# Optimization experiments

Measured on AMD Instinct MI355X. Metric: run time of the kernel, lower is better.

## Reference

```python
import jax, jax.numpy as jnp
import numpy as np

# Config (matches BlockConfig defaults for linear attention)
B, S, D = 2, 4096, 2048
H, KVH, HD, CK = 16, 8, 128, 4   # n_heads, n_kv_heads, head_dim, conv_kernel
DQK, DV = KVH * HD, H * HD       # 1024, 2048
EPS = 1e-6


def setup_inputs() -> dict:
    key = jax.random.key(0)
    ks = jax.random.split(key, 12)
    std = 0.02
    return {
        "x": jax.random.normal(ks[0], (B, S, D), jnp.float32),
        "wq": jax.random.normal(ks[1], (DQK, D), jnp.float32) * std,
        "wk": jax.random.normal(ks[2], (DQK, D), jnp.float32) * std,
        "wv": jax.random.normal(ks[3], (DV, D), jnp.float32) * std,
        "wo": jax.random.normal(ks[4], (D, DV), jnp.float32) * std,
        "q_conv_w": jax.random.normal(ks[5], (DQK, 1, CK), jnp.float32) * std,
        "k_conv_w": jax.random.normal(ks[6], (DQK, 1, CK), jnp.float32) * std,
        "alpha_w": jax.random.normal(ks[7], (H, D), jnp.float32) * std,
        "alpha_b": jnp.zeros((H,), jnp.float32),
        "beta_w": jax.random.normal(ks[8], (H, D), jnp.float32) * std,
        "beta_b": jnp.zeros((H,), jnp.float32),
        "g_w": jax.random.normal(ks[9], (DV, D), jnp.float32) * std,
        "norm_q_w": jnp.ones((HD,), jnp.float32),
        "norm_k_w": jnp.ones((HD,), jnp.float32),
    }


def _rmsnorm(x, w):
    # normalize over last dim (head_dim) in fp32, elementwise affine, no bias
    xf = x.astype(jnp.float32)
    var = jnp.mean(xf * xf, axis=-1, keepdims=True)
    return (w * xf * jax.lax.rsqrt(var + EPS)).astype(x.dtype)


def _causal_dwconv(x, w):
    # x: (B, S, C); w: (C, 1, k) depthwise; torch Conv1d padding=k-1 then [:S]
    # == left-pad (k-1, 0) cross-correlation
    y = jax.lax.conv_general_dilated(
        x.transpose(0, 2, 1), w, window_strides=(1,),
        padding=[(CK - 1, 0)], feature_group_count=w.shape[0],
        dimension_numbers=("NCH", "OIH", "NCH"))
    return y.transpose(0, 2, 1)


def reference(x, wq, wk, wv, wo, q_conv_w, k_conv_w,
              alpha_w, alpha_b, beta_w, beta_b, g_w, norm_q_w, norm_k_w):
    Q = x @ wq.T                              # (B,S,DQK)
    K = x @ wk.T                              # (B,S,DQK)
    V = x @ wv.T                              # (B,S,DV)
    Q = _causal_dwconv(Q, q_conv_w)
    K = _causal_dwconv(K, k_conv_w)
    Q = _rmsnorm(Q.reshape(B, S, KVH, HD), norm_q_w)
    K = _rmsnorm(K.reshape(B, S, KVH, HD), norm_k_w)
    V = V.reshape(B, S, H, HD)
    alpha = jax.nn.sigmoid(x @ alpha_w.T + alpha_b)              # (B,S,H)
    beta = jax.nn.sigmoid(x @ beta_w.T + beta_b) / (HD ** 0.5)   # (B,S,H)
    rep = H // KVH
    Q = jnp.repeat(Q, rep, axis=2)            # (B,S,H,HD)
    K = jnp.repeat(K, rep, axis=2)

    # time-major for scan
    Qt = Q.transpose(1, 0, 2, 3)
    Kt = K.transpose(1, 0, 2, 3)
    Vt = V.transpose(1, 0, 2, 3)
    at = alpha.transpose(1, 0, 2)
    bt = beta.transpose(1, 0, 2)

    S0 = jnp.zeros((B, H, HD, HD), x.dtype)

    def step(S_state, inp):
        q_t, k_t, v_t, a_t, b_t = inp
        pred = jnp.einsum("bhd,bhdv->bhv", k_t, S_state)
        delta = v_t - pred
        update = jnp.einsum("bhv,bhd->bhdv", delta, k_t)
        S_state = a_t[:, :, None, None] * S_state + b_t[:, :, None, None] * update
        o_t = jnp.einsum("bhd,bhdv->bhv", q_t, S_state)
        return S_state, o_t

    _, O = jax.lax.scan(step, S0, (Qt, Kt, Vt, at, bt))  # O: (S,B,H,HD)
    out = O.transpose(1, 0, 2, 3).reshape(B, S, DV)
    g = jax.nn.sigmoid(x @ g_w.T)
    return (g * out) @ wo.T
```

## Files before the change

### kernel.cpp

```cpp
#include <hip/hip_runtime.h>
#include <stdint.h>

#define DEV static __device__ __forceinline__

typedef __bf16 bf16x8 __attribute__((ext_vector_type(8)));
typedef float f32x4 __attribute__((ext_vector_type(4)));

constexpr int Bc = 2, Sc = 4096, Dc = 2048, Hc = 16, KVHc = 8, HDc = 128;
constexpr int DQKc = 1024, DVc = 2048;
constexpr int Mc = Bc * Sc;
constexpr int NCATc = 6144;
constexpr int CT = 64;
constexpr int NCH = Sc / CT;
constexpr int COEF_STRIDE = 25088;
constexpr float EPSc = 1e-6f;

DEV uint16_t f2bf(float f) {
  uint32_t u = __float_as_uint(f);
  u += 0x7FFFu + ((u >> 16) & 1u);
  return (uint16_t)(u >> 16);
}
DEV float bf2f(uint16_t h) { return __uint_as_float(((uint32_t)h) << 16); }
DEV float sigmoidf_(float z) { return 1.0f / (1.0f + __expf(-z)); }

DEV void unpack8(uint4 u, float* f) {
  f[0] = __uint_as_float(u.x << 16); f[1] = __uint_as_float(u.x & 0xFFFF0000u);
  f[2] = __uint_as_float(u.y << 16); f[3] = __uint_as_float(u.y & 0xFFFF0000u);
  f[4] = __uint_as_float(u.z << 16); f[5] = __uint_as_float(u.z & 0xFFFF0000u);
  f[6] = __uint_as_float(u.w << 16); f[7] = __uint_as_float(u.w & 0xFFFF0000u);
}

DEV void gload16(void* lds, const void* g) {
  auto gp = (const __attribute__((address_space(1))) uint32_t*)(uintptr_t)g;
  auto lp = (__attribute__((address_space(3))) uint32_t*)(uint32_t)(uintptr_t)lds;
  __builtin_amdgcn_global_load_lds(gp, lp, 16, 0, 0);
}

DEV void sync_lds() {
  asm volatile("s_waitcnt lgkmcnt(0)" ::: "memory");
  __builtin_amdgcn_sched_barrier(0);
  __builtin_amdgcn_s_barrier();
  __builtin_amdgcn_sched_barrier(0);
}

__global__ __launch_bounds__(256) void cast6_kernel(const float* __restrict__ x,
                                                    const float* __restrict__ wq,
                                                    const float* __restrict__ wk,
                                                    const float* __restrict__ wv,
                                                    const float* __restrict__ gw,
                                                    const float* __restrict__ wo,
                                                    uint16_t* __restrict__ xb,
                                                    uint16_t* __restrict__ wcat,
                                                    uint16_t* __restrict__ wob) {
  int i = blockIdx.x * blockDim.x + threadIdx.x;
  const int stride = gridDim.x * blockDim.x;
  for (; i < 8388608; i += stride) {
    const float* src;
    uint16_t* dst;
    int off;
    if (i < 4194304)      { src = x;  dst = xb;                     off = i; }
    else if (i < 4718592) { src = wq; dst = wcat;                   off = i - 4194304; }
    else if (i < 5242880) { src = wk; dst = wcat + DQKc * Dc;       off = i - 4718592; }
    else if (i < 6291456) { src = wv; dst = wcat + 2 * DQKc * Dc;   off = i - 5242880; }
    else if (i < 7340032) { src = gw; dst = wcat + 2 * DQKc * Dc + DVc * Dc; off = i - 6291456; }
    else                  { src = wo; dst = wob;                    off = i - 7340032; }
    float4 v = *(const float4*)(src + (size_t)off * 4);
    ushort4 o;
    o.x = f2bf(v.x); o.y = f2bf(v.y); o.z = f2bf(v.z); o.w = f2bf(v.w);
    *(ushort4*)(dst + (size_t)off * 4) = o;
  }
}

template <typename OutT>
__global__ __launch_bounds__(512, 2) void gemm256_bt(const uint16_t* __restrict__ A,
                                                     const uint16_t* __restrict__ Bw,
                                                     OutT* __restrict__ C, int Ndim, int Kdim,
                                                     int lda) {
  __shared__ uint16_t sT[2][2][2][8192];

  const int nbn = Ndim / 256;
  const int cpx = nbn >> 3;
  const int xcd = blockIdx.x & 7, lin = blockIdx.x >> 3;
  const int bn = xcd * cpx + lin % cpx;
  const int bm = lin / cpx;

  const int tid = threadIdx.x;
  const int wid = tid >> 6, lane = tid & 63;
  const int wm = wid >> 2, wn = wid & 3;
  const int lr = lane & 15;
  const int sswz8 = (((lane >> 4) ^ ((lr >> 1) & 3)) * 8);
  const int arow_base = wm * 128 + lr;
  const int brow_base = wn * 64 + lr;

  const uint16_t* Ab = A + (size_t)(bm * 256) * lda;
  const uint16_t* Bb = Bw + (size_t)(bn * 256) * Kdim;
  const int NT = Kdim >> 6;

  int srowA[2];
  int soff[2];
  const int wbase = tid & ~63;
#pragma unroll
  for (int u = 0; u < 2; ++u) {
    int L = u * 512 + tid;
    srowA[u] = L >> 2;
    soff[u] = (((L & 3) ^ ((L >> 3) & 3)) * 8);
  }

  auto STAGE = [&](int buf, int mat, int kh, int kt) {
    const uint16_t* gb = mat == 0 ? Ab : Bb;
    const int ld = mat == 0 ? lda : Kdim;
    uint16_t* rg = &sT[buf][mat][kh][0];
#pragma unroll
    for (int u = 0; u < 2; ++u) {
      const uint16_t* g = gb + (size_t)srowA[u] * ld + kt * 64 + kh * 32 + soff[u];
      gload16(rg + (u * 512 + wbase) * 8, g);
    }
  };

  f32x4 acc[8][4] = {};
  bf16x8 bfr[4];

  STAGE(0, 0, 0, 0); STAGE(0, 1, 0, 0);
  STAGE(0, 0, 1, 0); STAGE(0, 1, 1, 0);
  STAGE(1, 0, 0, 1); STAGE(1, 1, 0, 1);
  asm volatile("s_waitcnt vmcnt(4)" ::: "memory");
  __builtin_amdgcn_s_barrier();

  for (int kt = 0; kt < NT; ++kt) {
    const int buf = kt & 1;
    const uint16_t* aR0 = &sT[buf][0][0][0];
    const uint16_t* bR0 = &sT[buf][1][0][0];
    const uint16_t* aR1 = &sT[buf][0][1][0];
    const uint16_t* bR1 = &sT[buf][1][1][0];

    {
      bf16x8 af[4];
#pragma unroll
      for (int m = 0; m < 4; ++m)
        af[m] = *(const bf16x8*)&aR0[(arow_base + m * 16) * 32 + sswz8];
#pragma unroll
      for (int n = 0; n < 4; ++n)
        bfr[n] = *(const bf16x8*)&bR0[(brow_base + n * 16) * 32 + sswz8];
      if (kt + 1 < NT) STAGE(buf ^ 1, 0, 1, kt + 1);
      __builtin_amdgcn_s_setprio(1);
#pragma unroll
      for (int m = 0; m < 4; ++m)
#pragma unroll
        for (int n = 0; n < 4; ++n)
          acc[m][n] = __builtin_amdgcn_mfma_f32_16x16x32_bf16(af[m], bfr[n], acc[m][n], 0, 0, 0);
      __builtin_amdgcn_s_setprio(0);
      __builtin_amdgcn_s_barrier();
    }
    {
      bf16x8 af[4];
#pragma unroll
      for (int m = 0; m < 4; ++m)
        af[m] = *(const bf16x8*)&aR0[(arow_base + (m + 4) * 16) * 32 + sswz8];
      if (kt + 1 < NT) STAGE(buf ^ 1, 1, 1, kt + 1);
      __builtin_amdgcn_s_setprio(1);
#pragma unroll
      for (int m = 0; m < 4; ++m)
#pragma unroll
        for (int n = 0; n < 4; ++n)
          acc[m + 4][n] = __builtin_amdgcn_mfma_f32_16x16x32_bf16(af[m], bfr[n], acc[m + 4][n], 0, 0, 0);
      __builtin_amdgcn_s_setprio(0);
      __builtin_amdgcn_s_barrier();
    }
    {
      bf16x8 af[4];
#pragma unroll
      for (int m = 0; m < 4; ++m)
        af[m] = *(const bf16x8*)&aR1[(arow_base + m * 16) * 32 + sswz8];
#pragma unroll
      for (int n = 0; n < 4; ++n)
        bfr[n] = *(const bf16x8*)&bR1[(brow_base + n * 16) * 32 + sswz8];
      if (kt + 2 < NT) STAGE(buf, 0, 0, kt + 2);
      __builtin_amdgcn_s_setprio(1);
#pragma unroll
      for (int m = 0; m < 4; ++m)
#pragma unroll
        for (int n = 0; n < 4; ++n)
          acc[m][n] = __builtin_amdgcn_mfma_f32_16x16x32_bf16(af[m], bfr[n], acc[m][n], 0, 0, 0);
      __builtin_amdgcn_s_setprio(0);
      __builtin_amdgcn_s_barrier();
    }
    {
      bf16x8 af[4];
#pragma unroll
      for (int m = 0; m < 4; ++m)
        af[m] = *(const bf16x8*)&aR1[(arow_base + (m + 4) * 16) * 32 + sswz8];
      if (kt + 2 < NT) STAGE(buf, 1, 0, kt + 2);
      __builtin_amdgcn_s_setprio(1);
#pragma unroll
      for (int m = 0; m < 4; ++m)
#pragma unroll
        for (int n = 0; n < 4; ++n)
          acc[m + 4][n] = __builtin_amdgcn_mfma_f32_16x16x32_bf16(af[m], bfr[n], acc[m + 4][n], 0, 0, 0);
      __builtin_amdgcn_s_setprio(0);
    }
    if (kt + 1 < NT) {
      if (kt + 2 < NT)
        asm volatile("s_waitcnt vmcnt(4)" ::: "memory");
      else
        asm volatile("s_waitcnt vmcnt(0)" ::: "memory");
      __builtin_amdgcn_s_barrier();
    }
  }

  const int r0 = (lane >> 4) * 4;
#pragma unroll
  for (int m = 0; m < 8; ++m)
#pragma unroll
    for (int n = 0; n < 4; ++n) {
      int col = bn * 256 + wn * 64 + n * 16 + lr;
#pragma unroll
      for (int j = 0; j < 4; ++j) {
        int row = bm * 256 + wm * 128 + m * 16 + r0 + j;
        float val = acc[m][n][j];
        if constexpr (sizeof(OutT) == 2)
          C[(size_t)row * Ndim + col] = (OutT)f2bf(val);
        else
          C[(size_t)row * Ndim + col] = (OutT)val;
      }
    }
}

__global__ __launch_bounds__(256) void alphabeta_kernel(const float* __restrict__ x,
                                                        const float* __restrict__ aw,
                                                        const float* __restrict__ abias,
                                                        const float* __restrict__ bw,
                                                        const float* __restrict__ bbias,
                                                        float* __restrict__ out) {
  __shared__ float xs[4 * Dc];
  const int row0 = blockIdx.x * 4;
  const float* xp = x + (size_t)row0 * Dc;
  for (int i = threadIdx.x; i < 4 * Dc / 4; i += 256)
    *(float4*)&xs[i * 4] = *(const float4*)(xp + (size_t)i * 4);
  __syncthreads();
  const int o = threadIdx.x >> 3, lg = threadIdx.x & 7;
  const float* wrow = (o < 16) ? (aw + (size_t)o * Dc) : (bw + (size_t)(o - 16) * Dc);
  float s0 = 0.f, s1 = 0.f, s2 = 0.f, s3 = 0.f;
  for (int k = lg * 4; k < Dc; k += 32) {
    float4 wv = *(const float4*)(wrow + k);
    float4 x0 = *(const float4*)&xs[k];
    float4 x1 = *(const float4*)&xs[Dc + k];
    float4 x2 = *(const float4*)&xs[2 * Dc + k];
    float4 x3 = *(const float4*)&xs[3 * Dc + k];
    s0 += x0.x * wv.x + x0.y * wv.y + x0.z * wv.z + x0.w * wv.w;
    s1 += x1.x * wv.x + x1.y * wv.y + x1.z * wv.z + x1.w * wv.w;
    s2 += x2.x * wv.x + x2.y * wv.y + x2.z * wv.z + x2.w * wv.w;
    s3 += x3.x * wv.x + x3.y * wv.y + x3.z * wv.z + x3.w * wv.w;
  }
#pragma unroll
  for (int m = 1; m < 8; m <<= 1) {
    s0 += __shfl_xor(s0, m); s1 += __shfl_xor(s1, m);
    s2 += __shfl_xor(s2, m); s3 += __shfl_xor(s3, m);
  }
  if (lg == 0) {
    float bias = (o < 16) ? abias[o] : bbias[o - 16];
    float scale = (o >= 16) ? 0.08838834764831845f : 1.0f;
    out[(size_t)(row0 + 0) * 32 + o] = sigmoidf_(s0 + bias) * scale;
    out[(size_t)(row0 + 1) * 32 + o] = sigmoidf_(s1 + bias) * scale;
    out[(size_t)(row0 + 2) * 32 + o] = sigmoidf_(s2 + bias) * scale;
    out[(size_t)(row0 + 3) * 32 + o] = sigmoidf_(s3 + bias) * scale;
  }
}

__global__ __launch_bounds__(256) void scores_kernel(const uint16_t* __restrict__ C1,
                                                     const float* __restrict__ qcw,
                                                     const float* __restrict__ kcw,
                                                     const float* __restrict__ nqw,
                                                     const float* __restrict__ nkw,
                                                     const float* __restrict__ ab,
                                                     uint8_t* __restrict__ coef,
                                                     uint16_t* __restrict__ Qn,
                                                     uint16_t* __restrict__ Kn) {
  __shared__ __align__(16) char smem[137728];
  uint16_t* sK = (uint16_t*)smem;
  uint16_t* sQ = (uint16_t*)(smem + 17408);
  uint16_t* sF = (uint16_t*)smem;
  uint16_t* sM2 = (uint16_t*)(smem + 18432);
  float* Lb = (float*)(smem + 108544);
  float* bbv = Lb + 128;
  uint16_t* Ktg = (uint16_t*)(smem + 109568);
  uint16_t* Et = (uint16_t*)(smem + 128000);
  float* gCb = (float*)(smem + 137216);

  auto Wt_p  = [&](int hd) { return (float*)(smem + hd * 17408); };
  auto Msh_p = [&](int hd) { return (uint16_t*)(smem + 34816 + hd * 18432); };
  auto Msl_p = [&](int hd) { return (uint16_t*)(smem + 44032 + hd * 18432); };
  auto Thh_p = [&](int hd) { return (uint16_t*)(smem + 71680 + hd * 18432); };
  auto Thl_p = [&](int hd) { return (uint16_t*)(smem + 80896 + hd * 18432); };

  const int bid = blockIdx.x;
  const int c = bid & 63, kh = (bid >> 6) & 7, b = bid >> 9;
  const int t0 = c * 64;
  const int tid = threadIdx.x;
  const int w = tid >> 6, l = tid & 63, lr = l & 15, lk = (l >> 4) * 8;
  const int sr = tid >> 2, sq2 = tid & 3;

  auto cb_p = [&](int hd) {
    return coef + (size_t)((b * Hc + kh * 2 + hd) * NCH + c) * COEF_STRIDE;
  };

  {
    const int ch0 = sq2 * 32;
    const int t = t0 + sr;
    float qa[32], ka[32];
    float sqs = 0.f, sks = 0.f;
#pragma unroll
    for (int u = 0; u < 4; ++u) {
      uint4 qt[4], kt4[4];
#pragma unroll
      for (int j = 0; j < 4; ++j) {
        int tt = t - 3 + j;
        if (tt >= 0) {
          size_t rbj = (size_t)(b * Sc + tt) * NCATc + kh * HDc + ch0 + u * 8;
          qt[j] = *(const uint4*)(C1 + rbj);
          kt4[j] = *(const uint4*)(C1 + rbj + 1024);
        } else {
          qt[j] = make_uint4(0, 0, 0, 0);
          kt4[j] = make_uint4(0, 0, 0, 0);
        }
      }
      float qf[4][8], kf[4][8];
#pragma unroll
      for (int j = 0; j < 4; ++j) { unpack8(qt[j], qf[j]); unpack8(kt4[j], kf[j]); }
#pragma unroll
      for (int e = 0; e < 8; ++e) {
        const int ch = kh * HDc + ch0 + u * 8 + e;
        float4 wq4 = *(const float4*)(qcw + ch * 4);
        float4 wk4 = *(const float4*)(kcw + ch * 4);
        float qv = qf[0][e] * wq4.x + qf[1][e] * wq4.y + qf[2][e] * wq4.z + qf[3][e] * wq4.w;
        float kv = kf[0][e] * wk4.x + kf[1][e] * wk4.y + kf[2][e] * wk4.z + kf[3][e] * wk4.w;
        qa[u * 8 + e] = qv; ka[u * 8 + e] = kv;
        sqs += qv * qv; sks += kv * kv;
      }
    }
    sqs += __shfl_xor(sqs, 1); sqs += __shfl_xor(sqs, 2);
    sks += __shfl_xor(sks, 1); sks += __shfl_xor(sks, 2);
    const float rq = rsqrtf(sqs * (1.f / HDc) + EPSc);
    const float rk = rsqrtf(sks * (1.f / HDc) + EPSc);
    const size_t gq = (size_t)(b * Sc + t) * DQKc + kh * HDc + ch0;
#pragma unroll
    for (int u = 0; u < 4; ++u) {
      uint32_t qpk[4], kpk[4];
#pragma unroll
      for (int p = 0; p < 4; ++p) {
        const int e = u * 8 + p * 2;
        const int cc = ch0 + e;
        uint16_t q0 = f2bf(nqw[cc] * qa[e] * rq);
        uint16_t q1 = f2bf(nqw[cc + 1] * qa[e + 1] * rq);
        uint16_t k0 = f2bf(nkw[cc] * ka[e] * rk);
        uint16_t k1 = f2bf(nkw[cc + 1] * ka[e + 1] * rk);
        qpk[p] = (uint32_t)q0 | ((uint32_t)q1 << 16);
        kpk[p] = (uint32_t)k0 | ((uint32_t)k1 << 16);
      }
      uint4 qv4 = make_uint4(qpk[0], qpk[1], qpk[2], qpk[3]);
      uint4 kv4 = make_uint4(kpk[0], kpk[1], kpk[2], kpk[3]);
      *(uint4*)&sQ[sr * 136 + ch0 + u * 8] = qv4;
      *(uint4*)&sK[sr * 136 + ch0 + u * 8] = kv4;
      *(uint4*)(Qn + gq + u * 8) = qv4;
      *(uint4*)(Kn + gq + u * 8) = kv4;
    }
  }
  if (tid < 128) {
    const int hd = tid >> 6, tt = tid & 63;
    const float* abp = ab + (size_t)(b * Sc + t0 + tt) * 32 + (kh * 2 + hd);
    float av = fmaxf(abp[0], 1e-30f);
    float bv = abp[16];
    float la = log2f(av);
    float L = la;
#pragma unroll
    for (int off = 1; off < 64; off <<= 1) {
      float up = __shfl_up(L, off, 64);
      if (tt >= off) L += up;
    }
    Lb[hd * 64 + tt] = L; bbv[hd * 64 + tt] = bv;
    float* gout = (float*)(cb_p(hd) + 24576);
    gout[tt] = exp2f(L - la);
    gout[64 + tt] = exp2f(L);
  }
  __syncthreads();

  f32x4 kkacc[4] = {}, qkacc[4] = {};
#pragma unroll
  for (int k0 = 0; k0 < 128; k0 += 32) {
    bf16x8 ka = *(const bf16x8*)&sK[(16 * w + lr) * 136 + k0 + lk];
    bf16x8 qa = *(const bf16x8*)&sQ[(16 * w + lr) * 136 + k0 + lk];
#pragma unroll
    for (int n = 0; n < 4; ++n) {
      bf16x8 kb = *(const bf16x8*)&sK[(16 * n + lr) * 136 + k0 + lk];
      kkacc[n] = __builtin_amdgcn_mfma_f32_16x16x32_bf16(ka, kb, kkacc[n], 0, 0, 0);
      qkacc[n] = __builtin_amdgcn_mfma_f32_16x16x32_bf16(qa, kb, qkacc[n], 0, 0, 0);
    }
  }
  __syncthreads();

  {
#pragma unroll
    for (int u = 0; u < 4; ++u) {
      uint4 kd = *(const uint4*)&sK[sr * 136 + sq2 * 32 + u * 8];
      const int c0 = sq2 * 32 + u * 8;
      const int tsw = sr ^ (sq2 << 4);
      uint32_t x0 = kd.x, x1 = kd.y, x2 = kd.z, x3 = kd.w;
      Ktg[(c0 + 0) * 72 + tsw] = (uint16_t)x0; Ktg[(c0 + 1) * 72 + tsw] = (uint16_t)(x0 >> 16);
      Ktg[(c0 + 2) * 72 + tsw] = (uint16_t)x1; Ktg[(c0 + 3) * 72 + tsw] = (uint16_t)(x1 >> 16);
      Ktg[(c0 + 4) * 72 + tsw] = (uint16_t)x2; Ktg[(c0 + 5) * 72 + tsw] = (uint16_t)(x2 >> 16);
      Ktg[(c0 + 6) * 72 + tsw] = (uint16_t)x3; Ktg[(c0 + 7) * 72 + tsw] = (uint16_t)(x3 >> 16);
    }
    if (tid < 128) {
      const int hd = tid >> 6, tt = tid & 63;
      gCb[hd * 64 + tt] = exp2f(Lb[hd * 64 + 63] - Lb[hd * 64 + tt]) * bbv[hd * 64 + tt];
    }
  }
  __syncthreads();

#pragma unroll
  for (int hd = 0; hd < 2; ++hd) {
    float* Wt = Wt_p(hd);
    uint16_t* Mh = Msh_p(hd);
    uint16_t* Ml = Msl_p(hd);
    const float* Lh = Lb + hd * 64;
    const float* bh = bbv + hd * 64;
#pragma unroll
    for (int n = 0; n < 4; ++n)
#pragma unroll
      for (int jj = 0; jj < 4; ++jj) {
        const int i = 16 * w + (l >> 4) * 4 + jj;
        const int j = 16 * n + lr;
        float Li = Lh[i];
        float Lim = (i > 0) ? Lh[(i > 0) ? i - 1 : 0] : 0.f;
        float Lj = Lh[j];
        float bj = bh[j];
        float wv = (j < i) ? exp2f(Lim - Lj) * bj * kkacc[n][jj] : 0.f;
        Wt[j * 68 + i] = wv;
        float ms = (j <= i) ? exp2f(Li - Lj) * bj * qkacc[n][jj] : 0.f;
        uint16_t mh = f2bf(ms);
        Mh[i * 72 + j] = mh;
        Ml[i * 72 + j] = f2bf(ms - bf2f(mh));
      }
  }
  __syncthreads();

  if (tid < 128) {
    const int hd = tid >> 6, col = tid & 63;
    float* Wt = Wt_p(hd);
    uint16_t* Th = Thh_p(hd);
    uint16_t* Tl = Thl_p(hd);
    float acc[64];
#pragma unroll
    for (int i = 0; i < 64; ++i) acc[i] = 0.f;
#pragma unroll
    for (int ll = 0; ll < 64; ++ll) {
      float xl = ((col == ll) ? 1.f : 0.f) - acc[ll];
      uint16_t xh = f2bf(xl);
      Th[col * 72 + ll] = xh;
      Tl[col * 72 + ll] = f2bf(xl - bf2f(xh));
#pragma unroll
      for (int i = ll + 1; i < 64; ++i)
        acc[i] = fmaf(Wt[ll * 68 + i], xl, acc[i]);
    }
  }
  __syncthreads();

  for (int hd = 0; hd < 2; ++hd) {
    uint16_t* Mh = Msh_p(hd);
    uint16_t* Ml = Msl_p(hd);
    uint16_t* Th = Thh_p(hd);
    uint16_t* Tl = Thl_p(hd);
    uint16_t* m2out = (uint16_t*)cb_p(hd);
    uint16_t* fout = (uint16_t*)cb_p(hd) + 4096;

    {
      const int j2 = tid >> 2, tq = tid & 3;
#pragma unroll
      for (int p = 0; p < 16; ++p) {
        int t1 = tq * 16 + p;
        float ev = gCb[hd * 64 + t1] * (bf2f(Th[j2 * 72 + t1]) + bf2f(Tl[j2 * 72 + t1]));
        Et[j2 * 72 + t1] = f2bf(ev);
      }
    }
    __syncthreads();

    f32x4 m2acc[4] = {};
#pragma unroll
    for (int k0 = 0; k0 < 64; k0 += 32) {
      bf16x8 ah = *(const bf16x8*)&Mh[(16 * w + lr) * 72 + k0 + lk];
      bf16x8 al = *(const bf16x8*)&Ml[(16 * w + lr) * 72 + k0 + lk];
#pragma unroll
      for (int n = 0; n < 4; ++n) {
        bf16x8 bhf = *(const bf16x8*)&Th[(16 * n + lr) * 72 + k0 + lk];
        bf16x8 blf = *(const bf16x8*)&Tl[(16 * n + lr) * 72 + k0 + lk];
        m2acc[n] = __builtin_amdgcn_mfma_f32_16x16x32_bf16(ah, bhf, m2acc[n], 0, 0, 0);
        m2acc[n] = __builtin_amdgcn_mfma_f32_16x16x32_bf16(ah, blf, m2acc[n], 0, 0, 0);
        m2acc[n] = __builtin_amdgcn_mfma_f32_16x16x32_bf16(al, bhf, m2acc[n], 0, 0, 0);
      }
    }
    f32x4 facc[2][4] = {};
#pragma unroll
    for (int k0 = 0; k0 < 64; k0 += 32) {
      bf16x8 eb[4];
#pragma unroll
      for (int n = 0; n < 4; ++n)
        eb[n] = *(const bf16x8*)&Et[(16 * n + lr) * 72 + k0 + lk];
      const int ksw = (k0 + lk) ^ (w << 4);
      bf16x8 ka0 = *(const bf16x8*)&Ktg[(32 * w + lr) * 72 + ksw];
      bf16x8 ka1 = *(const bf16x8*)&Ktg[(32 * w + 16 + lr) * 72 + ksw];
#pragma unroll
      for (int n = 0; n < 4; ++n) {
        facc[0][n] = __builtin_amdgcn_mfma_f32_16x16x32_bf16(ka0, eb[n], facc[0][n], 0, 0, 0);
        facc[1][n] = __builtin_amdgcn_mfma_f32_16x16x32_bf16(ka1, eb[n], facc[1][n], 0, 0, 0);
      }
    }
#pragma unroll
    for (int n = 0; n < 4; ++n)
#pragma unroll
      for (int jj = 0; jj < 4; ++jj) {
        const int i = 16 * w + (l >> 4) * 4 + jj;
        const int j = 16 * n + lr;
        sM2[i * 72 + j] = f2bf(m2acc[n][jj]);
        sF[(32 * w + (l >> 4) * 4 + jj) * 72 + j] = f2bf(facc[0][n][jj]);
        sF[(32 * w + 16 + (l >> 4) * 4 + jj) * 72 + j] = f2bf(facc[1][n][jj]);
      }
    __syncthreads();
    {
      const int i2 = tid >> 2, tq = tid & 3;
      uint4 a0 = *(const uint4*)&sM2[i2 * 72 + tq * 16];
      uint4 a1 = *(const uint4*)&sM2[i2 * 72 + tq * 16 + 8];
      *(uint4*)(m2out + i2 * 64 + ((2 * tq) ^ (i2 & 7)) * 8) = a0;
      *(uint4*)(m2out + i2 * 64 + ((2 * tq + 1) ^ (i2 & 7)) * 8) = a1;
#pragma unroll
      for (int e = 0; e < 4; ++e) {
        int L = tid * 4 + e;
        int rw = L >> 3, s = L & 7;
        *(uint4*)(fout + rw * 64 + (s ^ (rw & 7)) * 8) = *(const uint4*)&sF[rw * 72 + s * 8];
      }
    }
    __syncthreads();
  }
}

__global__ __launch_bounds__(256, 1) void scan_kernel(const uint16_t* __restrict__ Qn,
                                                      const uint16_t* __restrict__ Kn,
                                                      uint16_t* C1,
                                                      const uint8_t* __restrict__ coef) {
  __shared__ __align__(16) uint16_t Kb[64 * 136];
  __shared__ __align__(16) uint16_t Qb[64 * 136];
  __shared__ __align__(16) uint16_t M2b[2][64 * 64];
  __shared__ __align__(16) uint16_t Fb[2][128 * 64];
  __shared__ __align__(16) uint16_t Vb[64 * 24];
  __shared__ __align__(16) uint16_t Rt[16 * 72];
  __shared__ __align__(16) uint16_t Sh[16 * 136];
  __shared__ __align__(16) uint16_t Slo[16 * 136];
  __shared__ float gABb[128];

  const int bid = blockIdx.x;
  const int kh = bid & 7;
  const int j2 = bid >> 3;
  const int sl = j2 >> 2;
  const int b = (j2 >> 1) & 1;
  const int h = kh * 2 + (j2 & 1);
  const int ch0 = (b * Hc + h) * NCH;

  const int tid = threadIdx.x;
  const int w = tid >> 6, l = tid & 63;
  const int lr = l & 15, lk = (l >> 4) * 8;
  const int row0 = 16 * w + (l >> 4) * 4;
  const int vcol = lr;
  const int sr = tid >> 2, sq2 = tid & 3;
  const int wbase = tid & ~63;

  const size_t kqbase = (size_t)(b * Sc) * DQKc + kh * HDc;
  const size_t vbase = (size_t)(b * Sc) * NCATc + 2048 + h * HDc + sl * 16;
  uint16_t* Gb = C1 + (size_t)(b * Sc) * NCATc + 4096 + h * HDc + sl * 16 + vcol;

  float sreg[2][4] = {};
  uint4 kA[4], kB[4], qA[4], qB[4];
  ushort4 gv0, gv1;

  auto LOADS = [&](int cn, int nb, uint4 (&kd)[4], uint4 (&qd)[4],
                   uint4& vd, float& gd, ushort4& gvd) {
    const uint16_t* cf = (const uint16_t*)(coef + (size_t)(ch0 + cn) * COEF_STRIDE);
#pragma unroll
    for (int u = 0; u < 2; ++u)
      gload16(&M2b[nb][(u * 256 + wbase) * 8], cf + (size_t)(u * 256 + tid) * 8);
#pragma unroll
    for (int u = 0; u < 4; ++u)
      gload16(&Fb[nb][(u * 256 + wbase) * 8], cf + 4096 + (size_t)(u * 256 + tid) * 8);
    const size_t rb = kqbase + (size_t)(cn * CT + sr) * DQKc + sq2 * 32;
#pragma unroll
    for (int u = 0; u < 4; ++u) {
      kd[u] = *(const uint4*)(Kn + rb + u * 8);
      qd[u] = *(const uint4*)(Qn + rb + u * 8);
    }
    if (tid < 128) {
      vd = *(const uint4*)(C1 + vbase + (size_t)(cn * CT + (tid >> 1)) * NCATc + (tid & 1) * 8);
      gd = ((const float*)(cf + 12288))[tid];
    }
    const uint16_t* gpre = Gb + (size_t)(cn * CT) * NCATc;
    gvd.x = gpre[(size_t)(row0 + 0) * NCATc];
    gvd.y = gpre[(size_t)(row0 + 1) * NCATc];
    gvd.z = gpre[(size_t)(row0 + 2) * NCATc];
    gvd.w = gpre[(size_t)(row0 + 3) * NCATc];
  };
  auto WSTAGE = [&](const uint4 (&kd)[4], const uint4 (&qd)[4],
                    const uint4& vd, const float& gd) {
#pragma unroll
    for (int u = 0; u < 4; ++u) {
      *(uint4*)&Kb[sr * 136 + sq2 * 32 + u * 8] = kd[u];
      *(uint4*)&Qb[sr * 136 + sq2 * 32 + u * 8] = qd[u];
    }
    if (tid < 128) {
      *(uint4*)&Vb[(tid >> 1) * 24 + (tid & 1) * 8] = vd;
      gABb[tid] = gd;
    }
  };

  auto CHUNK = [&](int c, bool pre, uint4 (&kcur)[4], uint4 (&knxt)[4],
                   uint4 (&qcur)[4], uint4 (&qnxt)[4], ushort4& gvcur, ushort4& gvnxt) {
    uint4 vd; float gd = 0.f;
    if (pre) LOADS(c + 1, (c + 1) & 1, knxt, qnxt, vd, gd, gvnxt);
    const int cb = c & 1;

    f32x4 accP = {0, 0, 0, 0}, accPq = {0, 0, 0, 0};
#pragma unroll
    for (int k0 = 0; k0 < 128; k0 += 32) {
      bf16x8 ka = *(const bf16x8*)&Kb[(16 * w + lr) * 136 + k0 + lk];
      bf16x8 qa = *(const bf16x8*)&Qb[(16 * w + lr) * 136 + k0 + lk];
      bf16x8 shf = *(const bf16x8*)&Sh[lr * 136 + k0 + lk];
      bf16x8 slf = *(const bf16x8*)&Slo[lr * 136 + k0 + lk];
      accP = __builtin_amdgcn_mfma_f32_16x16x32_bf16(ka, shf, accP, 0, 0, 0);
      accP = __builtin_amdgcn_mfma_f32_16x16x32_bf16(ka, slf, accP, 0, 0, 0);
      accPq = __builtin_amdgcn_mfma_f32_16x16x32_bf16(qa, shf, accPq, 0, 0, 0);
      accPq = __builtin_amdgcn_mfma_f32_16x16x32_bf16(qa, slf, accPq, 0, 0, 0);
    }
    float gbv[4];
#pragma unroll
    for (int j = 0; j < 4; ++j) gbv[j] = gABb[64 + row0 + j];
    const float gT = gABb[127];
    {
      float rv[4];
#pragma unroll
      for (int j = 0; j < 4; ++j) {
        float vv = bf2f(Vb[(row0 + j) * 24 + vcol]);
        float ga = gABb[row0 + j];
        rv[j] = vv - ga * accP[j];
      }
      uint32_t r01 = (uint32_t)f2bf(rv[0]) | ((uint32_t)f2bf(rv[1]) << 16);
      uint32_t r23 = (uint32_t)f2bf(rv[2]) | ((uint32_t)f2bf(rv[3]) << 16);
      *(uint2*)&Rt[vcol * 72 + row0] = make_uint2(r01, r23);
    }
    sync_lds();

    f32x4 accO = {0, 0, 0, 0};
    f32x4 accY0 = {0, 0, 0, 0}, accY1 = {0, 0, 0, 0};
#pragma unroll
    for (int k0 = 0; k0 < 64; k0 += 32) {
      const int sw = ((((k0 >> 3) + (l >> 4)) ^ (lr & 7)) * 8);
      bf16x8 rb8 = *(const bf16x8*)&Rt[lr * 72 + k0 + lk];
      bf16x8 ma = *(const bf16x8*)&M2b[cb][(16 * w + lr) * 64 + sw];
      bf16x8 f0 = *(const bf16x8*)&Fb[cb][(32 * w + lr) * 64 + sw];
      bf16x8 f1 = *(const bf16x8*)&Fb[cb][(32 * w + 16 + lr) * 64 + sw];
      accO = __builtin_amdgcn_mfma_f32_16x16x32_bf16(ma, rb8, accO, 0, 0, 0);
      accY0 = __builtin_amdgcn_mfma_f32_16x16x32_bf16(f0, rb8, accY0, 0, 0, 0);
      accY1 = __builtin_amdgcn_mfma_f32_16x16x32_bf16(f1, rb8, accY1, 0, 0, 0);
    }
    {
      uint16_t* gp = Gb + (size_t)(c * CT) * NCATc;
      uint16_t gvv[4] = {gvcur.x, gvcur.y, gvcur.z, gvcur.w};
#pragma unroll
      for (int j = 0; j < 4; ++j) {
        float o = gbv[j] * accPq[j] + accO[j];
        float gg = sigmoidf_(bf2f(gvv[j]));
        gp[(size_t)(row0 + j) * NCATc] = f2bf(o * gg);
      }
    }
    {
      uint16_t hi[4], lo[4];
#pragma unroll
      for (int j = 0; j < 4; ++j) {
        float s = gT * sreg[0][j] + accY0[j];
        sreg[0][j] = s;
        hi[j] = f2bf(s);
        lo[j] = f2bf(s - bf2f(hi[j]));
      }
      const int dk0 = 32 * w + (l >> 4) * 4;
      *(uint2*)&Sh[vcol * 136 + dk0] =
          make_uint2((uint32_t)hi[0] | ((uint32_t)hi[1] << 16),
                     (uint32_t)hi[2] | ((uint32_t)hi[3] << 16));
      *(uint2*)&Slo[vcol * 136 + dk0] =
          make_uint2((uint32_t)lo[0] | ((uint32_t)lo[1] << 16),
                     (uint32_t)lo[2] | ((uint32_t)lo[3] << 16));
    }
    {
      uint16_t hi[4], lo[4];
#pragma unroll
      for (int j = 0; j < 4; ++j) {
        float s = gT * sreg[1][j] + accY1[j];
        sreg[1][j] = s;
        hi[j] = f2bf(s);
        lo[j] = f2bf(s - bf2f(hi[j]));
      }
      const int dk0 = 32 * w + 16 + (l >> 4) * 4;
      *(uint2*)&Sh[vcol * 136 + dk0] =
          make_uint2((uint32_t)hi[0] | ((uint32_t)hi[1] << 16),
                     (uint32_t)hi[2] | ((uint32_t)hi[3] << 16));
      *(uint2*)&Slo[vcol * 136 + dk0] =
          make_uint2((uint32_t)lo[0] | ((uint32_t)lo[1] << 16),
                     (uint32_t)lo[2] | ((uint32_t)lo[3] << 16));
    }
    if (pre) WSTAGE(knxt, qnxt, vd, gd);
    __syncthreads();
  };

  {
    uint4 vd; float gd = 0.f;
    LOADS(0, 0, kA, qA, vd, gd, gv0);
    WSTAGE(kA, qA, vd, gd);
  }
  for (int i = tid; i < 16 * 136; i += 256) { Sh[i] = 0; Slo[i] = 0; }
  __syncthreads();

  for (int c2 = 0; c2 < NCH; c2 += 2) {
    CHUNK(c2, true, kA, kB, qA, qB, gv0, gv1);
    CHUNK(c2 + 1, c2 + 2 < NCH, kB, kA, qB, qA, gv1, gv0);
  }
}

extern "C" void kernel_launch(void* const* d_in, const int* in_sizes, int n_in,
                              void* d_out, int out_size, void* d_ws, size_t ws_size,
                              hipStream_t stream) {
  (void)in_sizes; (void)n_in; (void)out_size; (void)ws_size;
  const float* x     = (const float*)d_in[0];
  const float* wq    = (const float*)d_in[1];
  const float* wk    = (const float*)d_in[2];
  const float* wv    = (const float*)d_in[3];
  const float* wo    = (const float*)d_in[4];
  const float* qcw   = (const float*)d_in[5];
  const float* kcw   = (const float*)d_in[6];
  const float* aw    = (const float*)d_in[7];
  const float* abias = (const float*)d_in[8];
  const float* bw    = (const float*)d_in[9];
  const float* bbias = (const float*)d_in[10];
  const float* gw    = (const float*)d_in[11];
  const float* nqw   = (const float*)d_in[12];
  const float* nkw   = (const float*)d_in[13];

  uint8_t* ws = (uint8_t*)d_ws;
  uint16_t* xb   = (uint16_t*)(ws);
  uint16_t* wcat = (uint16_t*)(ws + 33554432);
  uint16_t* wob  = (uint16_t*)(ws + 58720256);
  uint16_t* c1   = (uint16_t*)(ws + 67108864);
  float*    abuf = (float*)   (ws + 167772160);
  uint16_t* qn   = (uint16_t*)(ws + 168820736);
  uint16_t* kn   = (uint16_t*)(ws + 185597952);
  uint8_t*  cofs = (uint8_t*)ws;

  cast6_kernel<<<2048, 256, 0, stream>>>(x, wq, wk, wv, gw, wo, xb, wcat, wob);
  gemm256_bt<uint16_t><<<768, 512, 0, stream>>>(xb, wcat, c1, NCATc, Dc, Dc);
  alphabeta_kernel<<<2048, 256, 0, stream>>>(x, aw, abias, bw, bbias, abuf);
  scores_kernel<<<1024, 256, 0, stream>>>(c1, qcw, kcw, nqw, nkw, abuf, cofs, qn, kn);
  scan_kernel<<<256, 256, 0, stream>>>(qn, kn, c1, cofs);
  gemm256_bt<float><<<256, 512, 0, stream>>>(c1 + 4096, wob, (float*)d_out, DVc, Dc, NCATc);
}
```

Measured before the change: 684.5 us.

## Split scan value columns across twice as many blocks, keep K/Q fragments in registers

Each scan block now handles 8 value columns instead of 16, so the grid doubles from 256 to 512 blocks with launch bounds allowing two blocks per CU. The K and Q tiles are loaded straight into registers in MFMA fragment layout rather than staged through LDS, which removes the Kb/Qb shared buffers and their write/read traffic. The cost is that half the lanes in the 16-wide MFMA column dimension are idle (zero-padded Rt), and every block redundantly loads K, Q and the coefficient matrices, doubling that global traffic.

```diff
diff --git a/kernel.cpp b/kernel.cpp
--- a/kernel.cpp
+++ b/kernel.cpp
@@ -541,15 +541,13 @@
   }
 }
 
-__global__ __launch_bounds__(256, 1) void scan_kernel(const uint16_t* __restrict__ Qn,
+__global__ __launch_bounds__(256, 2) void scan_kernel(const uint16_t* __restrict__ Qn,
                                                       const uint16_t* __restrict__ Kn,
                                                       uint16_t* C1,
                                                       const uint8_t* __restrict__ coef) {
-  __shared__ __align__(16) uint16_t Kb[64 * 136];
-  __shared__ __align__(16) uint16_t Qb[64 * 136];
   __shared__ __align__(16) uint16_t M2b[2][64 * 64];
   __shared__ __align__(16) uint16_t Fb[2][128 * 64];
-  __shared__ __align__(16) uint16_t Vb[64 * 24];
+  __shared__ __align__(16) uint16_t Vb[64 * 12];
   __shared__ __align__(16) uint16_t Rt[16 * 72];
   __shared__ __align__(16) uint16_t Sh[16 * 136];
   __shared__ __align__(16) uint16_t Slo[16 * 136];
@@ -568,12 +566,11 @@
   const int lr = l & 15, lk = (l >> 4) * 8;
   const int row0 = 16 * w + (l >> 4) * 4;
   const int vcol = lr;
-  const int sr = tid >> 2, sq2 = tid & 3;
   const int wbase = tid & ~63;
 
   const size_t kqbase = (size_t)(b * Sc) * DQKc + kh * HDc;
-  const size_t vbase = (size_t)(b * Sc) * NCATc + 2048 + h * HDc + sl * 16;
-  uint16_t* Gb = C1 + (size_t)(b * Sc) * NCATc + 4096 + h * HDc + sl * 16 + vcol;
+  const size_t vbase = (size_t)(b * Sc) * NCATc + 2048 + h * HDc + sl * 8;
+  uint16_t* Gb = C1 + (size_t)(b * Sc) * NCATc + 4096 + h * HDc + sl * 8 + vcol;
 
   float sreg[2][4] = {};
   uint4 kA[4], kB[4], qA[4], qB[4];
@@ -588,33 +585,29 @@
 #pragma unroll
     for (int u = 0; u < 4; ++u)
       gload16(&Fb[nb][(u * 256 + wbase) * 8], cf + 4096 + (size_t)(u * 256 + tid) * 8);
-    const size_t rb = kqbase + (size_t)(cn * CT + sr) * DQKc + sq2 * 32;
+    const size_t frow = kqbase + (size_t)(cn * CT + 16 * w + lr) * DQKc + lk;
 #pragma unroll
     for (int u = 0; u < 4; ++u) {
-      kd[u] = *(const uint4*)(Kn + rb + u * 8);
-      qd[u] = *(const uint4*)(Qn + rb + u * 8);
-    }
-    if (tid < 128) {
-      vd = *(const uint4*)(C1 + vbase + (size_t)(cn * CT + (tid >> 1)) * NCATc + (tid & 1) * 8);
+      kd[u] = *(const uint4*)(Kn + frow + u * 32);
+      qd[u] = *(const uint4*)(Qn + frow + u * 32);
+    }
+    if (tid < 64)
+      vd = *(const uint4*)(C1 + vbase + (size_t)(cn * CT + tid) * NCATc);
+    if (tid < 128)
       gd = ((const float*)(cf + 12288))[tid];
-    }
-    const uint16_t* gpre = Gb + (size_t)(cn * CT) * NCATc;
-    gvd.x = gpre[(size_t)(row0 + 0) * NCATc];
-    gvd.y = gpre[(size_t)(row0 + 1) * NCATc];
-    gvd.z = gpre[(size_t)(row0 + 2) * NCATc];
-    gvd.w = gpre[(size_t)(row0 + 3) * NCATc];
+    if (vcol < 8) {
+      const uint16_t* gpre = Gb + (size_t)(cn * CT) * NCATc;
+      gvd.x = gpre[(size_t)(row0 + 0) * NCATc];
+      gvd.y = gpre[(size_t)(row0 + 1) * NCATc];
+      gvd.z = gpre[(size_t)(row0 + 2) * NCATc];
+      gvd.w = gpre[(size_t)(row0 + 3) * NCATc];
+    } else {
+      gvd = make_ushort4(0, 0, 0, 0);
+    }
   };
-  auto WSTAGE = [&](const uint4 (&kd)[4], const uint4 (&qd)[4],
-                    const uint4& vd, const float& gd) {
-#pragma unroll
-    for (int u = 0; u < 4; ++u) {
-      *(uint4*)&Kb[sr * 136 + sq2 * 32 + u * 8] = kd[u];
-      *(uint4*)&Qb[sr * 136 + sq2 * 32 + u * 8] = qd[u];
-    }
-    if (tid < 128) {
-      *(uint4*)&Vb[(tid >> 1) * 24 + (tid & 1) * 8] = vd;
-      gABb[tid] = gd;
-    }
+  auto WSTAGE = [&](const uint4& vd, const float& gd) {
+    if (tid < 64) *(uint4*)&Vb[tid * 12] = vd;
+    if (tid < 128) gABb[tid] = gd;
   };
 
   auto CHUNK = [&](int c, bool pre, uint4 (&kcur)[4], uint4 (&knxt)[4],
@@ -625,11 +618,11 @@
 
     f32x4 accP = {0, 0, 0, 0}, accPq = {0, 0, 0, 0};
 #pragma unroll
-    for (int k0 = 0; k0 < 128; k0 += 32) {
-      bf16x8 ka = *(const bf16x8*)&Kb[(16 * w + lr) * 136 + k0 + lk];
-      bf16x8 qa = *(const bf16x8*)&Qb[(16 * w + lr) * 136 + k0 + lk];
-      bf16x8 shf = *(const bf16x8*)&Sh[lr * 136 + k0 + lk];
-      bf16x8 slf = *(const bf16x8*)&Slo[lr * 136 + k0 + lk];
+    for (int u = 0; u < 4; ++u) {
+      bf16x8 ka = *(const bf16x8*)&kcur[u];
+      bf16x8 qa = *(const bf16x8*)&qcur[u];
+      bf16x8 shf = *(const bf16x8*)&Sh[lr * 136 + u * 32 + lk];
+      bf16x8 slf = *(const bf16x8*)&Slo[lr * 136 + u * 32 + lk];
       accP = __builtin_amdgcn_mfma_f32_16x16x32_bf16(ka, shf, accP, 0, 0, 0);
       accP = __builtin_amdgcn_mfma_f32_16x16x32_bf16(ka, slf, accP, 0, 0, 0);
       accPq = __builtin_amdgcn_mfma_f32_16x16x32_bf16(qa, shf, accPq, 0, 0, 0);
@@ -639,11 +632,11 @@
 #pragma unroll
     for (int j = 0; j < 4; ++j) gbv[j] = gABb[64 + row0 + j];
     const float gT = gABb[127];
-    {
+    if (vcol < 8) {
       float rv[4];
 #pragma unroll
       for (int j = 0; j < 4; ++j) {
-        float vv = bf2f(Vb[(row0 + j) * 24 + vcol]);
+        float vv = bf2f(Vb[(row0 + j) * 12 + vcol]);
         float ga = gABb[row0 + j];
         rv[j] = vv - ga * accP[j];
       }
@@ -666,7 +659,7 @@
       accY0 = __builtin_amdgcn_mfma_f32_16x16x32_bf16(f0, rb8, accY0, 0, 0, 0);
       accY1 = __builtin_amdgcn_mfma_f32_16x16x32_bf16(f1, rb8, accY1, 0, 0, 0);
     }
-    {
+    if (vcol < 8) {
       uint16_t* gp = Gb + (size_t)(c * CT) * NCATc;
       uint16_t gvv[4] = {gvcur.x, gvcur.y, gvcur.z, gvcur.w};
 #pragma unroll
@@ -676,7 +669,7 @@
         gp[(size_t)(row0 + j) * NCATc] = f2bf(o * gg);
       }
     }
-    {
+    if (vcol < 8) {
       uint16_t hi[4], lo[4];
 #pragma unroll
       for (int j = 0; j < 4; ++j) {
@@ -692,34 +685,33 @@
       *(uint2*)&Slo[vcol * 136 + dk0] =
           make_uint2((uint32_t)lo[0] | ((uint32_t)lo[1] << 16),
                      (uint32_t)lo[2] | ((uint32_t)lo[3] << 16));
-    }
-    {
-      uint16_t hi[4], lo[4];
+      uint16_t hi1[4], lo1[4];
 #pragma unroll
       for (int j = 0; j < 4; ++j) {
         float s = gT * sreg[1][j] + accY1[j];
         sreg[1][j] = s;
-        hi[j] = f2bf(s);
-        lo[j] = f2bf(s - bf2f(hi[j]));
-      }
-      const int dk0 = 32 * w + 16 + (l >> 4) * 4;
-      *(uint2*)&Sh[vcol * 136 + dk0] =
-          make_uint2((uint32_t)hi[0] | ((uint32_t)hi[1] << 16),
-                     (uint32_t)hi[2] | ((uint32_t)hi[3] << 16));
-      *(uint2*)&Slo[vcol * 136 + dk0] =
-          make_uint2((uint32_t)lo[0] | ((uint32_t)lo[1] << 16),
-                     (uint32_t)lo[2] | ((uint32_t)lo[3] << 16));
-    }
-    if (pre) WSTAGE(knxt, qnxt, vd, gd);
+        hi1[j] = f2bf(s);
+        lo1[j] = f2bf(s - bf2f(hi1[j]));
+      }
+      const int dk1 = 32 * w + 16 + (l >> 4) * 4;
+      *(uint2*)&Sh[vcol * 136 + dk1] =
+          make_uint2((uint32_t)hi1[0] | ((uint32_t)hi1[1] << 16),
+                     (uint32_t)hi1[2] | ((uint32_t)hi1[3] << 16));
+      *(uint2*)&Slo[vcol * 136 + dk1] =
+          make_uint2((uint32_t)lo1[0] | ((uint32_t)lo1[1] << 16),
+                     (uint32_t)lo1[2] | ((uint32_t)lo1[3] << 16));
+    }
+    if (pre) WSTAGE(vd, gd);
     __syncthreads();
   };
 
   {
     uint4 vd; float gd = 0.f;
     LOADS(0, 0, kA, qA, vd, gd, gv0);
-    WSTAGE(kA, qA, vd, gd);
+    WSTAGE(vd, gd);
   }
   for (int i = tid; i < 16 * 136; i += 256) { Sh[i] = 0; Slo[i] = 0; }
+  for (int i = tid; i < 16 * 72; i += 256) Rt[i] = 0;
   __syncthreads();
 
   for (int c2 = 0; c2 < NCH; c2 += 2) {
@@ -761,6 +753,6 @@
   gemm256_bt<uint16_t><<<768, 512, 0, stream>>>(xb, wcat, c1, NCATc, Dc, Dc);
   alphabeta_kernel<<<2048, 256, 0, stream>>>(x, aw, abias, bw, bbias, abuf);
   scores_kernel<<<1024, 256, 0, stream>>>(c1, qcw, kcw, nqw, nkw, abuf, cofs, qn, kn);
-  scan_kernel<<<256, 256, 0, stream>>>(qn, kn, c1, cofs);
+  scan_kernel<<<512, 256, 0, stream>>>(qn, kn, c1, cofs);
   gemm256_bt<float><<<256, 512, 0, stream>>>(c1 + 4096, wob, (float*)d_out, DVc, Dc, NCATc);
 }
```

Result: slower. 698.6 us (+2.1%).
